# Performance work log

Measured on AMD Instinct MI355X. Metric: run time of the kernel, lower is better.

## Reference

```python
import jax, jax.numpy as jnp
import numpy as np

GH, GW, B, H, OUT = 9, 9, 1024, 256, 1


def setup_inputs() -> dict:
    key = jax.random.key(0)
    ks = jax.random.split(key, 16)
    N = GH * GW
    s3 = 1.0 / np.sqrt(3 * H)
    sH = 1.0 / np.sqrt(H)
    return {
        "x": jax.random.normal(ks[0], (B, GH, GW), jnp.float32),
        "h_ext": jax.random.normal(ks[1], (B, H), jnp.float32),
        "c_ext": jax.random.normal(ks[2], (B, H), jnp.float32),
        "grid_h": jax.random.normal(ks[3], (GH, GW, B, H), jnp.float32),
        "grid_c": jax.random.normal(ks[4], (GH, GW, B, H), jnp.float32),
        "W_hp": jax.random.normal(ks[5], (N, H, 3 * H), jnp.float32) * s3,
        "b_hp": jax.random.normal(ks[6], (N, H), jnp.float32) * s3,
        "W_cp": jax.random.normal(ks[7], (N, H, 3 * H), jnp.float32) * s3,
        "b_cp": jax.random.normal(ks[8], (N, H), jnp.float32) * s3,
        "W_ih": jax.random.normal(ks[9], (N, 4 * H, 1), jnp.float32) * sH,
        "W_hh": jax.random.normal(ks[10], (N, 4 * H, H), jnp.float32) * sH,
        "b_ih": jax.random.normal(ks[11], (N, 4 * H), jnp.float32) * sH,
        "b_hh": jax.random.normal(ks[12], (N, 4 * H), jnp.float32) * sH,
        "W_out": jax.random.normal(ks[13], (OUT, H), jnp.float32) * sH,
        "b_out": jnp.zeros((OUT,), jnp.float32),
    }


def _lstm_cell(x_cell, h0, c0, W_ih_k, W_hh_k, b_ih_k, b_hh_k):
    # x_cell: [B,1], h0/c0: [B,H]; torch LSTMCell math
    gates = x_cell @ W_ih_k.T + b_ih_k + h0 @ W_hh_k.T + b_hh_k  # [B,4H]
    i, f, g, o = jnp.split(gates, 4, axis=1)
    i, f, o = jax.nn.sigmoid(i), jax.nn.sigmoid(f), jax.nn.sigmoid(o)
    g = jnp.tanh(g)
    c = f * c0 + i * g
    h = o * jnp.tanh(c)
    return h, c


def reference(x, h_ext, c_ext, grid_h, grid_c,
              W_hp, b_hp, W_cp, b_cp,
              W_ih, W_hh, b_ih, b_hh, W_out, b_out):
    zeros = jnp.zeros((B, H), x.dtype)
    # new states, updated in raster order; left/up neighbors read NEW states
    new_h = [[None] * GW for _ in range(GH)]
    new_c = [[None] * GW for _ in range(GH)]
    for i in range(GH):
        for j in range(GW):
            k = i * GW + j
            h_prev, c_prev = grid_h[i, j], grid_c[i, j]
            if i == 0 and j == 0:
                h_left, c_left = h_ext, c_ext
            elif j > 0:
                h_left, c_left = new_h[i][j - 1], new_c[i][j - 1]
            else:
                h_left, c_left = zeros, zeros
            if i > 0:
                h_up, c_up = new_h[i - 1][j], new_c[i - 1][j]
            else:
                h_up, c_up = zeros, zeros
            comb_h = jnp.concatenate([h_left, h_up, h_prev], axis=1)  # [B,3H]
            comb_c = jnp.concatenate([c_left, c_up, c_prev], axis=1)
            ph = comb_h @ W_hp[k].T + b_hp[k]
            pc = comb_c @ W_cp[k].T + b_cp[k]
            x_cell = x[:, i, j][:, None]  # [B,1]
            h_new, c_new = _lstm_cell(x_cell, ph, pc, W_ih[k], W_hh[k], b_ih[k], b_hh[k])
            new_h[i][j], new_c[i][j] = h_new, c_new
    final_h, final_c = new_h[-1][-1], new_c[-1][-1]
    # fc_out with fc_layers_out=[0]: Linear + ReLU, then sigmoid
    out = jax.nn.sigmoid(jax.nn.relu(final_h @ W_out.T + b_out))
    gh = jnp.stack([jnp.stack(r, 0) for r in new_h], 0)
    gc = jnp.stack([jnp.stack(r, 0) for r in new_c], 0)
    return out, final_h, final_c, gh, gc
```

## Files before the change

kernel.cpp:

```cpp
#include <hip/hip_runtime.h>
#include <math.h>

#define BATCH 1024
#define HID 256
#define W3 768
#define SLOT (BATCH * HID)

typedef __bf16 bf16_t;
typedef __bf16 bf16x8 __attribute__((ext_vector_type(8)));
typedef __bf16 bf16x4 __attribute__((ext_vector_type(4)));
typedef float f32x4 __attribute__((ext_vector_type(4)));

__device__ inline bf16x8 cvt8(const float4 a, const float4 b) {
    bf16x8 r;
    r[0] = (bf16_t)a.x; r[1] = (bf16_t)a.y; r[2] = (bf16_t)a.z; r[3] = (bf16_t)a.w;
    r[4] = (bf16_t)b.x; r[5] = (bf16_t)b.y; r[6] = (bf16_t)b.z; r[7] = (bf16_t)b.w;
    return r;
}
__device__ inline bf16x4 cvt4(const float4 a) {
    bf16x4 r;
    r[0] = (bf16_t)a.x; r[1] = (bf16_t)a.y; r[2] = (bf16_t)a.z; r[3] = (bf16_t)a.w;
    return r;
}

__device__ inline int swz_work(int bid, int N) {
    const int xcd = bid & 7, idx = bid >> 3;
    const int q = N >> 3, r = N & 7;
    return (xcd < r ? xcd * (q + 1) : r * (q + 1) + (xcd - r) * q) + idx;
}

__global__ __launch_bounds__(256) void wcp_conv(
        const float* __restrict__ wcp, bf16_t* __restrict__ wcpb) {
    const size_t n4 = (size_t)81 * HID * W3 / 4;
    size_t i = (size_t)blockIdx.x * 256 + threadIdx.x;
    const size_t nth = (size_t)gridDim.x * 256;
    for (; i < n4; i += nth) {
        const float4 v = *(const float4*)(wcp + i * 4);
        *(bf16x4*)(wcpb + i * 4) = cvt4(v);
    }
}

__global__ __launch_bounds__(256) void whp_t_kernel(
        const float* __restrict__ whp, bf16_t* __restrict__ whpT) {
    const int k = blockIdx.z;
    const int m0 = blockIdx.x * 64, u0 = blockIdx.y * 64;
    const int t = threadIdx.x;
    const int tm = t & 63, tg = t >> 6;
    const float* src = whp + (size_t)k * HID * W3;
    bf16_t* dst = whpT + (size_t)k * W3 * HID;
    #pragma unroll
    for (int c = 0; c < 2; ++c) {
        const int ub = u0 + (tg + c * 4) * 8;
        bf16x8 v;
        #pragma unroll
        for (int i = 0; i < 8; ++i)
            v[i] = (bf16_t)src[(size_t)(ub + i) * W3 + m0 + tm];
        *(bf16x8*)(dst + (size_t)(m0 + tm) * HID + ub) = v;
    }
}

__global__ __launch_bounds__(256) void gvec_kernel(
        const float* __restrict__ Whh, const float* __restrict__ bhp,
        const float* __restrict__ bih, const float* __restrict__ bhh,
        float* __restrict__ gvec) {
    const int k = blockIdx.x, t = threadIdx.x;
    __shared__ float bsm[HID];
    bsm[t] = bhp[(size_t)k * HID + t];
    __syncthreads();
    #pragma unroll
    for (int g = 0; g < 4; ++g) {
        const int n4 = g * HID + t;
        const float* wr = Whh + (size_t)k * 4 * HID * HID + (size_t)n4 * HID;
        float s = 0.f;
        for (int u = 0; u < HID; u += 4) {
            const float4 w = *(const float4*)(wr + u);
            s += w.x * bsm[u] + w.y * bsm[u + 1] + w.z * bsm[u + 2] + w.w * bsm[u + 3];
        }
        gvec[(size_t)k * 1024 + n4] = s + bih[(size_t)k * 1024 + n4]
                                        + bhh[(size_t)k * 1024 + n4];
    }
}

__global__ __launch_bounds__(256) void compose_kernel(
        const float* __restrict__ Whh, const bf16_t* __restrict__ WhpT,
        bf16_t* __restrict__ CC) {
    __shared__ bf16_t As[128][40];
    __shared__ bf16_t Bs[128][40];
    const int work = swz_work(blockIdx.x, gridDim.x);
    const int k = work / 48, inner = work % 48;
    const int mt = inner % 6, by = inner / 6;
    const int m0 = mt * 128;
    const int t = threadIdx.x;
    const int lane = t & 63, wid = t >> 6;
    const int wm = wid & 1, wn = wid >> 1;
    const int ln = lane & 15, lh = lane >> 4;
    const int sr = t >> 1, sq = (t & 1) * 16;
    const int g_r = sr >> 5, du_r = sr & 31;
    const float* arow = Whh + (size_t)k * 1024 * HID
                        + (size_t)(g_r * HID + by * 32 + du_r) * HID + sq;
    const bf16_t* brow = WhpT + (size_t)k * W3 * HID + (size_t)(m0 + sr) * HID + sq;

    f32x4 acc[4][4] = {};
    for (int kb = 0; kb < 8; ++kb) {
        const float4 a0 = *(const float4*)(arow + kb * 32);
        const float4 a1 = *(const float4*)(arow + kb * 32 + 4);
        const float4 a2 = *(const float4*)(arow + kb * 32 + 8);
        const float4 a3 = *(const float4*)(arow + kb * 32 + 12);
        const bf16x8 bv0 = *(const bf16x8*)(brow + kb * 32);
        const bf16x8 bv1 = *(const bf16x8*)(brow + kb * 32 + 8);
        const bf16x8 av0 = cvt8(a0, a1), av1 = cvt8(a2, a3);
        __syncthreads();
        *(bf16x8*)&As[sr][sq] = av0;
        *(bf16x8*)&As[sr][sq + 8] = av1;
        *(bf16x8*)&Bs[sr][sq] = bv0;
        *(bf16x8*)&Bs[sr][sq + 8] = bv1;
        __syncthreads();
        bf16x8 af[4], bfv[4];
        #pragma unroll
        for (int mf = 0; mf < 4; ++mf)
            af[mf] = *(const bf16x8*)&Bs[wm * 64 + mf * 16 + ln][lh * 8];
        #pragma unroll
        for (int cf = 0; cf < 4; ++cf)
            bfv[cf] = *(const bf16x8*)&As[wn * 64 + cf * 16 + ln][lh * 8];
        #pragma unroll
        for (int mf = 0; mf < 4; ++mf)
            #pragma unroll
            for (int cf = 0; cf < 4; ++cf)
                acc[mf][cf] = __builtin_amdgcn_mfma_f32_16x16x32_bf16(
                    af[mf], bfv[cf], acc[mf][cf], 0, 0, 0);
    }
    bf16_t* outp = CC + (size_t)k * 1024 * W3;
    #pragma unroll
    for (int cf = 0; cf < 4; ++cf) {
        const int c = by * 128 + wn * 64 + cf * 16 + ln;
        #pragma unroll
        for (int mf = 0; mf < 4; ++mf) {
            const int m = m0 + wm * 64 + mf * 16 + lh * 4;
            bf16x4 v;
            #pragma unroll
            for (int r = 0; r < 4; ++r) v[r] = (bf16_t)acc[mf][cf][r];
            *(bf16x4*)(outp + (size_t)c * W3 + m) = v;
        }
    }
}

__global__ __launch_bounds__(256) void prevgates_kernel(
        const float* __restrict__ gridh, const float* __restrict__ gridc,
        const bf16_t* __restrict__ CC, const bf16_t* __restrict__ Wcpb,
        const float* __restrict__ gvec, const float* __restrict__ Wih,
        const float* __restrict__ bcp, const float* __restrict__ x,
        bf16_t* __restrict__ GP, bf16_t* __restrict__ PP) {
    __shared__ bf16_t A1[128][40];
    __shared__ bf16_t A2[128][40];
    __shared__ bf16_t B1[128][40];
    __shared__ bf16_t B2[32][40];
    const int work = swz_work(blockIdx.x, gridDim.x);
    const int k = work >> 6, inner = work & 63;
    const int bx = inner & 7, by = inner >> 3;
    const int t = threadIdx.x;
    const int lane = t & 63, wid = t >> 6;
    const int wm = wid & 1, wn = wid >> 1;
    const int ln = lane & 15, lh = lane >> 4;
    const int b0 = bx * 128, u0 = by * 32;
    const int sr = t >> 1, sq = (t & 1) * 16;
    const int du2 = t >> 3, kk4 = (t & 7) * 4;

    const float* ha = gridh + (size_t)k * SLOT + (size_t)(b0 + sr) * HID + sq;
    const float* ca = gridc + (size_t)k * SLOT + (size_t)(b0 + sr) * HID + sq;
    const bf16_t* b1r = CC + (size_t)k * 1024 * W3 + (size_t)(by * 128 + sr) * W3 + 512 + sq;
    const bf16_t* b2r = Wcpb + (size_t)k * HID * W3 + (size_t)(u0 + du2) * W3 + 512 + kk4;

    f32x4 accg[4][4] = {};
    f32x4 accp[4] = {};
    for (int kb = 0; kb < 8; ++kb) {
        const float4 h0 = *(const float4*)(ha + kb * 32);
        const float4 h1 = *(const float4*)(ha + kb * 32 + 4);
        const float4 h2 = *(const float4*)(ha + kb * 32 + 8);
        const float4 h3 = *(const float4*)(ha + kb * 32 + 12);
        const float4 c0 = *(const float4*)(ca + kb * 32);
        const float4 c1 = *(const float4*)(ca + kb * 32 + 4);
        const float4 c2 = *(const float4*)(ca + kb * 32 + 8);
        const float4 c3 = *(const float4*)(ca + kb * 32 + 12);
        const bf16x8 w0 = *(const bf16x8*)(b1r + kb * 32);
        const bf16x8 w1 = *(const bf16x8*)(b1r + kb * 32 + 8);
        const bf16x4 p0 = *(const bf16x4*)(b2r + kb * 32);
        const bf16x8 hv0 = cvt8(h0, h1), hv1 = cvt8(h2, h3);
        const bf16x8 cv0 = cvt8(c0, c1), cv1 = cvt8(c2, c3);
        __syncthreads();
        *(bf16x8*)&A1[sr][sq] = hv0;  *(bf16x8*)&A1[sr][sq + 8] = hv1;
        *(bf16x8*)&A2[sr][sq] = cv0;  *(bf16x8*)&A2[sr][sq + 8] = cv1;
        *(bf16x8*)&B1[sr][sq] = w0;   *(bf16x8*)&B1[sr][sq + 8] = w1;
        *(bf16x4*)&B2[du2][kk4] = p0;
        __syncthreads();
        bf16x8 af1[4], af2[4], bf1[4], bf2;
        #pragma unroll
        for (int mf = 0; mf < 4; ++mf) {
            af1[mf] = *(const bf16x8*)&A1[wm * 64 + mf * 16 + ln][lh * 8];
            af2[mf] = *(const bf16x8*)&A2[wm * 64 + mf * 16 + ln][lh * 8];
        }
        #pragma unroll
        for (int g = 0; g < 4; ++g)
            bf1[g] = *(const bf16x8*)&B1[g * 32 + wn * 16 + ln][lh * 8];
        bf2 = *(const bf16x8*)&B2[wn * 16 + ln][lh * 8];
        #pragma unroll
        for (int mf = 0; mf < 4; ++mf) {
            #pragma unroll
            for (int g = 0; g < 4; ++g)
                accg[mf][g] = __builtin_amdgcn_mfma_f32_16x16x32_bf16(
                    af1[mf], bf1[g], accg[mf][g], 0, 0, 0);
            accp[mf] = __builtin_amdgcn_mfma_f32_16x16x32_bf16(
                af2[mf], bf2, accp[mf], 0, 0, 0);
        }
    }

    const int u = u0 + wn * 16 + ln;
    float wv[4], gv[4];
    #pragma unroll
    for (int g = 0; g < 4; ++g) {
        const int n4 = g * HID + u;
        wv[g] = Wih[(size_t)k * 1024 + n4];
        gv[g] = gvec[(size_t)k * 1024 + n4];
    }
    const float bc = bcp[(size_t)k * HID + u];
    const int blk = by * 8 + bx;
    bf16_t* gpb = GP + (size_t)k * (BATCH * 1024) + (size_t)blk * 16384;
    bf16_t* ppb = PP + (size_t)k * SLOT + (size_t)blk * 4096;
    #pragma unroll
    for (int mf = 0; mf < 4; ++mf) {
        #pragma unroll
        for (int rp = 0; rp < 2; ++rp) {
            bf16x8 v;
            #pragma unroll
            for (int a = 0; a < 2; ++a) {
                const int r = rp * 2 + a;
                const int b = b0 + wm * 64 + mf * 16 + lh * 4 + r;
                const float xv = x[(size_t)b * 81 + k];
                #pragma unroll
                for (int g = 0; g < 4; ++g)
                    v[a * 4 + g] = (bf16_t)(accg[mf][g][r] + gv[g] + xv * wv[g]);
            }
            *(bf16x8*)(gpb + (size_t)(mf * 2 + rp) * 2048 + t * 8) = v;
        }
    }
    #pragma unroll
    for (int j = 0; j < 2; ++j) {
        bf16x8 v;
        #pragma unroll
        for (int h2 = 0; h2 < 2; ++h2) {
            const int mf = j * 2 + h2;
            #pragma unroll
            for (int r = 0; r < 4; ++r)
                v[h2 * 4 + r] = (bf16_t)(accp[mf][r] + bc);
        }
        *(bf16x8*)(ppb + (size_t)j * 2048 + t * 8) = v;
    }
}

struct Stage2Desc {
    const float* hs0; const float* cs0;
    const float* hs1; const float* cs1;
    const bf16_t* cc; const bf16_t* wcpb;
    const bf16_t* gp; const bf16_t* pp;
    float* gh; float* gc;
};
struct Stage2Args { Stage2Desc d[9]; };

__global__ __launch_bounds__(256) void stage2_kernel(Stage2Args args) {
    __shared__ bf16_t A1[128][40];
    __shared__ bf16_t A2[128][40];
    __shared__ bf16_t B1[128][40];
    __shared__ bf16_t B2[32][40];
    const int work = swz_work(blockIdx.x, gridDim.x);
    const int cell = work >> 6, inner = work & 63;
    const Stage2Desc sd = args.d[cell];
    const int bx = inner & 7, by = inner >> 3;
    const int t = threadIdx.x;
    const int lane = t & 63, wid = t >> 6;
    const int wm = wid & 1, wn = wid >> 1;
    const int ln = lane & 15, lh = lane >> 4;
    const int b0 = bx * 128, u0 = by * 32;
    const int sr = t >> 1, sq = (t & 1) * 16;
    const int du2 = t >> 3, kk4 = (t & 7) * 4;

    const int blk = by * 8 + bx;
    const bf16_t* gpb = sd.gp + (size_t)blk * 16384;
    const bf16_t* ppb = sd.pp + (size_t)blk * 4096;
    bf16x8 gpv[8], ppv[2];
    #pragma unroll
    for (int e = 0; e < 8; ++e)
        gpv[e] = *(const bf16x8*)(gpb + (size_t)e * 2048 + t * 8);
    #pragma unroll
    for (int j = 0; j < 2; ++j)
        ppv[j] = *(const bf16x8*)(ppb + (size_t)j * 2048 + t * 8);

    f32x4 accg[4][4] = {};
    f32x4 accp[4] = {};
    const float* hseg[2] = { sd.hs0, sd.hs1 };
    const float* cseg[2] = { sd.cs0, sd.cs1 };

    for (int s = 0; s < 2; ++s) {
        const float* hp = hseg[s];
        if (!hp) continue;
        const float* cp = cseg[s];
        const int ko = s * 256;
        const float* ha = hp + (size_t)(b0 + sr) * HID + sq;
        const float* ca = cp + (size_t)(b0 + sr) * HID + sq;
        const bf16_t* b1r = sd.cc + (size_t)(by * 128 + sr) * W3 + ko + sq;
        const bf16_t* b2r = sd.wcpb + (size_t)(u0 + du2) * W3 + ko + kk4;
        for (int kb = 0; kb < 8; ++kb) {
            const float4 h0 = *(const float4*)(ha + kb * 32);
            const float4 h1 = *(const float4*)(ha + kb * 32 + 4);
            const float4 h2 = *(const float4*)(ha + kb * 32 + 8);
            const float4 h3 = *(const float4*)(ha + kb * 32 + 12);
            const float4 c0 = *(const float4*)(ca + kb * 32);
            const float4 c1 = *(const float4*)(ca + kb * 32 + 4);
            const float4 c2 = *(const float4*)(ca + kb * 32 + 8);
            const float4 c3 = *(const float4*)(ca + kb * 32 + 12);
            const bf16x8 w0 = *(const bf16x8*)(b1r + kb * 32);
            const bf16x8 w1 = *(const bf16x8*)(b1r + kb * 32 + 8);
            const bf16x4 p0 = *(const bf16x4*)(b2r + kb * 32);
            const bf16x8 hv0 = cvt8(h0, h1), hv1 = cvt8(h2, h3);
            const bf16x8 cv0 = cvt8(c0, c1), cv1 = cvt8(c2, c3);
            __syncthreads();
            *(bf16x8*)&A1[sr][sq] = hv0;  *(bf16x8*)&A1[sr][sq + 8] = hv1;
            *(bf16x8*)&A2[sr][sq] = cv0;  *(bf16x8*)&A2[sr][sq + 8] = cv1;
            *(bf16x8*)&B1[sr][sq] = w0;   *(bf16x8*)&B1[sr][sq + 8] = w1;
            *(bf16x4*)&B2[du2][kk4] = p0;
            __syncthreads();
            bf16x8 af1[4], af2[4], bf1[4], bf2;
            #pragma unroll
            for (int mf = 0; mf < 4; ++mf) {
                af1[mf] = *(const bf16x8*)&A1[wm * 64 + mf * 16 + ln][lh * 8];
                af2[mf] = *(const bf16x8*)&A2[wm * 64 + mf * 16 + ln][lh * 8];
            }
            #pragma unroll
            for (int g = 0; g < 4; ++g)
                bf1[g] = *(const bf16x8*)&B1[g * 32 + wn * 16 + ln][lh * 8];
            bf2 = *(const bf16x8*)&B2[wn * 16 + ln][lh * 8];
            #pragma unroll
            for (int mf = 0; mf < 4; ++mf) {
                #pragma unroll
                for (int g = 0; g < 4; ++g)
                    accg[mf][g] = __builtin_amdgcn_mfma_f32_16x16x32_bf16(
                        af1[mf], bf1[g], accg[mf][g], 0, 0, 0);
                accp[mf] = __builtin_amdgcn_mfma_f32_16x16x32_bf16(
                    af2[mf], bf2, accp[mf], 0, 0, 0);
            }
        }
    }

    const int u = u0 + wn * 16 + ln;
    float pcv[4][4];
    #pragma unroll
    for (int j = 0; j < 2; ++j)
        #pragma unroll
        for (int h2 = 0; h2 < 2; ++h2)
            #pragma unroll
            for (int r = 0; r < 4; ++r)
                pcv[j * 2 + h2][r] = accp[j * 2 + h2][r] + (float)ppv[j][h2 * 4 + r];
    #pragma unroll
    for (int mf = 0; mf < 4; ++mf) {
        #pragma unroll
        for (int rp = 0; rp < 2; ++rp) {
            const bf16x8 v = gpv[mf * 2 + rp];
            #pragma unroll
            for (int a = 0; a < 2; ++a) {
                const int r = rp * 2 + a;
                const int b = b0 + wm * 64 + mf * 16 + lh * 4 + r;
                const float gi = accg[mf][0][r] + (float)v[a * 4 + 0];
                const float gf = accg[mf][1][r] + (float)v[a * 4 + 1];
                const float gg = accg[mf][2][r] + (float)v[a * 4 + 2];
                const float go = accg[mf][3][r] + (float)v[a * 4 + 3];
                const float pc = pcv[mf][r];
                const float i_ = 1.f / (1.f + expf(-gi));
                const float f_ = 1.f / (1.f + expf(-gf));
                const float o_ = 1.f / (1.f + expf(-go));
                const float g_ = tanhf(gg);
                const float cn = f_ * pc + i_ * g_;
                const float hn = o_ * tanhf(cn);
                sd.gh[(size_t)b * HID + u] = hn;
                sd.gc[(size_t)b * HID + u] = cn;
            }
        }
    }
}

__global__ __launch_bounds__(256) void final_kernel(
        const float* __restrict__ gh88, const float* __restrict__ gc88,
        const float* __restrict__ Wout, const float* __restrict__ bout,
        float* __restrict__ out, float* __restrict__ fh, float* __restrict__ fc) {
    const int tid = blockIdx.x * blockDim.x + threadIdx.x;
    const int nth = gridDim.x * blockDim.x;
    for (int idx = tid; idx < BATCH * HID; idx += nth) {
        fh[idx] = gh88[idx];
        fc[idx] = gc88[idx];
    }
    if (tid < BATCH) {
        float s = bout[0];
        for (int k = 0; k < HID; ++k) s += gh88[(size_t)tid * HID + k] * Wout[k];
        s = fmaxf(s, 0.f);
        out[tid] = 1.f / (1.f + expf(-s));
    }
}

template<bool ATOMIC>
__device__ __forceinline__ void proj_core(
        const float* __restrict__ src, const float* __restrict__ W, int koff,
        const float* __restrict__ bias, float* __restrict__ out,
        bf16_t (*Asm)[40], bf16_t (*Bsm)[40]) {
    const int t = threadIdx.x;
    const int lane = t & 63, wid = t >> 6;
    const int wm = wid & 1, wn = wid >> 1;
    const int ln = lane & 15, lh = lane >> 4;
    const int b0 = blockIdx.x * 128, n0 = blockIdx.y * 128;
    const int sr = t >> 1, sq = (t & 1) * 16;
    const float* arow = src + (size_t)(b0 + sr) * HID + sq;
    const float* wrow = W + (size_t)(n0 + sr) * W3 + koff + sq;
    f32x4 acc[4][4] = {};
    for (int kb = 0; kb < 8; ++kb) {
        const float4 a0 = *(const float4*)(arow + kb * 32);
        const float4 a1 = *(const float4*)(arow + kb * 32 + 4);
        const float4 a2 = *(const float4*)(arow + kb * 32 + 8);
        const float4 a3 = *(const float4*)(arow + kb * 32 + 12);
        const float4 w0 = *(const float4*)(wrow + kb * 32);
        const float4 w1 = *(const float4*)(wrow + kb * 32 + 4);
        const float4 w2 = *(const float4*)(wrow + kb * 32 + 8);
        const float4 w3 = *(const float4*)(wrow + kb * 32 + 12);
        const bf16x8 av0 = cvt8(a0, a1), av1 = cvt8(a2, a3);
        const bf16x8 bv0 = cvt8(w0, w1), bv1 = cvt8(w2, w3);
        __syncthreads();
        *(bf16x8*)&Asm[sr][sq] = av0;
        *(bf16x8*)&Asm[sr][sq + 8] = av1;
        *(bf16x8*)&Bsm[sr][sq] = bv0;
        *(bf16x8*)&Bsm[sr][sq + 8] = bv1;
        __syncthreads();
        bf16x8 af[4], bfv[4];
        #pragma unroll
        for (int mf = 0; mf < 4; ++mf)
            af[mf] = *(const bf16x8*)&Asm[wm * 64 + mf * 16 + ln][lh * 8];
        #pragma unroll
        for (int nf = 0; nf < 4; ++nf)
            bfv[nf] = *(const bf16x8*)&Bsm[wn * 64 + nf * 16 + ln][lh * 8];
        #pragma unroll
        for (int mf = 0; mf < 4; ++mf)
            #pragma unroll
            for (int nf = 0; nf < 4; ++nf)
                acc[mf][nf] = __builtin_amdgcn_mfma_f32_16x16x32_bf16(
                    af[mf], bfv[nf], acc[mf][nf], 0, 0, 0);
    }
    #pragma unroll
    for (int nf = 0; nf < 4; ++nf) {
        const int n = n0 + wn * 64 + nf * 16 + ln;
        const float bn = ATOMIC ? 0.f : bias[n];
        #pragma unroll
        for (int mf = 0; mf < 4; ++mf)
            #pragma unroll
            for (int r = 0; r < 4; ++r) {
                const int b = b0 + wm * 64 + mf * 16 + lh * 4 + r;
                if (ATOMIC)
                    unsafeAtomicAdd(out + (size_t)b * HID + n, acc[mf][nf][r]);
                else
                    out[(size_t)b * HID + n] = acc[mf][nf][r] + bn;
            }
    }
}

struct SegDesc { const float* src; const float* W; const float* bias; float* out; int koff; };
struct SegArgs { SegDesc d[36]; };

__global__ __launch_bounds__(256) void projseg_kernel(SegArgs a) {
    __shared__ bf16_t As[128][40];
    __shared__ bf16_t Bs[128][40];
    const SegDesc d = a.d[blockIdx.z];
    if (d.bias) proj_core<false>(d.src, d.W, d.koff, d.bias, d.out, As, Bs);
    else        proj_core<true>(d.src, d.W, d.koff, nullptr, d.out, As, Bs);
}

struct CellDesc {
    const float* ph; const float* pc;
    const float* Whh; const float* Wih; const float* bih; const float* bhh;
    const float* xcol;
    float* gh; float* gc;
};
struct CellBatchArgs { CellDesc d[9]; };

__global__ __launch_bounds__(256) void cell_kernel(CellBatchArgs args) {
    const CellDesc cd = args.d[blockIdx.z];
    __shared__ bf16_t Psm[128][40];
    __shared__ bf16_t Wsm[128][40];
    const int t = threadIdx.x;
    const int lane = t & 63, wid = t >> 6;
    const int wm = wid & 1, wn = wid >> 1;
    const int ln = lane & 15, lh = lane >> 4;
    const int b0 = blockIdx.x * 128;
    const int u0 = blockIdx.y * 32;
    const int sr = t >> 1, sq = (t & 1) * 16;
    const float* prow = cd.ph + (size_t)(b0 + sr) * HID + sq;
    const int cg = sr >> 5, cdu = sr & 31;
    const float* wrow = cd.Whh + (size_t)(cg * HID + u0 + cdu) * HID + sq;
    f32x4 acc[4][4] = {};
    for (int kb = 0; kb < 8; ++kb) {
        const float4 p0 = *(const float4*)(prow + kb * 32);
        const float4 p1 = *(const float4*)(prow + kb * 32 + 4);
        const float4 p2 = *(const float4*)(prow + kb * 32 + 8);
        const float4 p3 = *(const float4*)(prow + kb * 32 + 12);
        const float4 w0 = *(const float4*)(wrow + kb * 32);
        const float4 w1 = *(const float4*)(wrow + kb * 32 + 4);
        const float4 w2 = *(const float4*)(wrow + kb * 32 + 8);
        const float4 w3 = *(const float4*)(wrow + kb * 32 + 12);
        const bf16x8 pv0 = cvt8(p0, p1), pv1 = cvt8(p2, p3);
        const bf16x8 wv0 = cvt8(w0, w1), wv1 = cvt8(w2, w3);
        __syncthreads();
        *(bf16x8*)&Psm[sr][sq] = pv0;
        *(bf16x8*)&Psm[sr][sq + 8] = pv1;
        *(bf16x8*)&Wsm[sr][sq] = wv0;
        *(bf16x8*)&Wsm[sr][sq + 8] = wv1;
        __syncthreads();
        bf16x8 af[4], bfr[4];
        #pragma unroll
        for (int mf = 0; mf < 4; ++mf)
            af[mf] = *(const bf16x8*)&Psm[wm * 64 + mf * 16 + ln][lh * 8];
        #pragma unroll
        for (int g = 0; g < 4; ++g)
            bfr[g] = *(const bf16x8*)&Wsm[g * 32 + wn * 16 + ln][lh * 8];
        #pragma unroll
        for (int mf = 0; mf < 4; ++mf)
            #pragma unroll
            for (int g = 0; g < 4; ++g)
                acc[mf][g] = __builtin_amdgcn_mfma_f32_16x16x32_bf16(
                    af[mf], bfr[g], acc[mf][g], 0, 0, 0);
    }
    const int u = u0 + wn * 16 + ln;
    float wih[4], bsum[4];
    #pragma unroll
    for (int g = 0; g < 4; ++g) {
        const int n = g * HID + u;
        wih[g] = cd.Wih[n];
        bsum[g] = cd.bih[n] + cd.bhh[n];
    }
    #pragma unroll
    for (int mf = 0; mf < 4; ++mf)
        #pragma unroll
        for (int r = 0; r < 4; ++r) {
            const int b = b0 + wm * 64 + mf * 16 + lh * 4 + r;
            const float xv = cd.xcol[(size_t)b * 81];
            const float gi = acc[mf][0][r] + xv * wih[0] + bsum[0];
            const float gf = acc[mf][1][r] + xv * wih[1] + bsum[1];
            const float gg = acc[mf][2][r] + xv * wih[2] + bsum[2];
            const float go = acc[mf][3][r] + xv * wih[3] + bsum[3];
            const float i_ = 1.f / (1.f + expf(-gi));
            const float f_ = 1.f / (1.f + expf(-gf));
            const float o_ = 1.f / (1.f + expf(-go));
            const float g_ = tanhf(gg);
            const float c0 = cd.pc[(size_t)b * HID + u];
            const float cn = f_ * c0 + i_ * g_;
            const float hn = o_ * tanhf(cn);
            cd.gh[(size_t)b * HID + u] = hn;
            cd.gc[(size_t)b * HID + u] = cn;
        }
}

extern "C" void kernel_launch(void* const* d_in, const int* in_sizes, int n_in,
                              void* d_out, int out_size, void* d_ws, size_t ws_size,
                              hipStream_t stream) {
    const float* x      = (const float*)d_in[0];
    const float* h_ext  = (const float*)d_in[1];
    const float* c_ext  = (const float*)d_in[2];
    const float* grid_h = (const float*)d_in[3];
    const float* grid_c = (const float*)d_in[4];
    const float* W_hp   = (const float*)d_in[5];
    const float* b_hp   = (const float*)d_in[6];
    const float* W_cp   = (const float*)d_in[7];
    const float* b_cp   = (const float*)d_in[8];
    const float* W_ih   = (const float*)d_in[9];
    const float* W_hh   = (const float*)d_in[10];
    const float* b_ih   = (const float*)d_in[11];
    const float* b_hh   = (const float*)d_in[12];
    const float* W_out  = (const float*)d_in[13];
    const float* b_out  = (const float*)d_in[14];

    float* out = (float*)d_out;
    float* fh  = out + BATCH * 1;
    float* fc  = fh + SLOT;
    float* gh  = fc + SLOT;
    float* gc  = gh + (size_t)81 * SLOT;

    const size_t wt_b  = (size_t)81 * W3 * HID * 2;
    const size_t wcp_b = (size_t)81 * HID * W3 * 2;
    const size_t cc_b  = (size_t)81 * 1024 * W3 * 2;
    const size_t gp_b  = (size_t)81 * BATCH * 1024 * 2;
    const size_t pp_b  = (size_t)81 * SLOT * 2;
    const size_t gv_b  = (size_t)81 * 1024 * 4;
    const size_t need = wt_b + wcp_b + cc_b + gp_b + pp_b + gv_b;

    if (ws_size >= need) {
        char* p = (char*)d_ws;
        bf16_t* WhpT = (bf16_t*)p; p += wt_b;
        bf16_t* Wcpb = (bf16_t*)p; p += wcp_b;
        bf16_t* CC   = (bf16_t*)p; p += cc_b;
        bf16_t* GP   = (bf16_t*)p; p += gp_b;
        bf16_t* PP   = (bf16_t*)p; p += pp_b;
        float*  gvec = (float*)p;

        wcp_conv<<<dim3(2048), 256, 0, stream>>>(W_cp, Wcpb);
        whp_t_kernel<<<dim3(12, 4, 81), 256, 0, stream>>>(W_hp, WhpT);
        gvec_kernel<<<dim3(81), 256, 0, stream>>>(W_hh, b_hp, b_ih, b_hh, gvec);
        compose_kernel<<<dim3(81 * 48), 256, 0, stream>>>(W_hh, WhpT, CC);
        prevgates_kernel<<<dim3(81 * 64), 256, 0, stream>>>(
            grid_h, grid_c, CC, Wcpb, gvec, W_ih, b_cp, x, GP, PP);

        for (int d = 0; d <= 16; ++d) {
            const int i_lo = d > 8 ? d - 8 : 0;
            const int i_hi = d < 8 ? d : 8;
            const int nc = i_hi - i_lo + 1;
            Stage2Args sa{};
            for (int s = 0; s < nc; ++s) {
                const int i = i_lo + s, j = d - i;
                const int k = i * 9 + j;
                const float *hl = nullptr, *cl = nullptr, *hu = nullptr, *cu = nullptr;
                if (i == 0 && j == 0)      { hl = h_ext; cl = c_ext; }
                else if (j > 0)            { hl = gh + (size_t)(k - 1) * SLOT;
                                             cl = gc + (size_t)(k - 1) * SLOT; }
                if (i > 0)                 { hu = gh + (size_t)(k - 9) * SLOT;
                                             cu = gc + (size_t)(k - 9) * SLOT; }
                sa.d[s] = { hl, cl, hu, cu,
                            CC + (size_t)k * 1024 * W3,
                            Wcpb + (size_t)k * HID * W3,
                            GP + (size_t)k * BATCH * 1024,
                            PP + (size_t)k * SLOT,
                            gh + (size_t)k * SLOT, gc + (size_t)k * SLOT };
            }
            stage2_kernel<<<dim3(nc * 64), 256, 0, stream>>>(sa);
        }
    } else {
        float* ws = (float*)d_ws;
        for (int d = 0; d <= 16; ++d) {
            const int i_lo = d > 8 ? d - 8 : 0;
            const int i_hi = d < 8 ? d : 8;
            const int nc = i_hi - i_lo + 1;
            SegArgs base{}, inc{};
            CellBatchArgs ca{};
            int nb = 0, ni = 0;
            for (int s = 0; s < nc; ++s) {
                const int i = i_lo + s, j = d - i;
                const int k = i * 9 + j;
                float* oh = ws + (size_t)(2 * s) * SLOT;
                float* oc = oh + SLOT;
                const float* Wh = W_hp + (size_t)k * HID * W3;
                const float* Wc = W_cp + (size_t)k * HID * W3;
                base.d[nb++] = { grid_h + (size_t)k * SLOT, Wh, b_hp + (size_t)k * HID, oh, 512 };
                base.d[nb++] = { grid_c + (size_t)k * SLOT, Wc, b_cp + (size_t)k * HID, oc, 512 };
                if (i == 0 && j == 0) {
                    inc.d[ni++] = { h_ext, Wh, nullptr, oh, 0 };
                    inc.d[ni++] = { c_ext, Wc, nullptr, oc, 0 };
                } else if (j > 0) {
                    inc.d[ni++] = { gh + (size_t)(k - 1) * SLOT, Wh, nullptr, oh, 0 };
                    inc.d[ni++] = { gc + (size_t)(k - 1) * SLOT, Wc, nullptr, oc, 0 };
                }
                if (i > 0) {
                    inc.d[ni++] = { gh + (size_t)(k - 9) * SLOT, Wh, nullptr, oh, 256 };
                    inc.d[ni++] = { gc + (size_t)(k - 9) * SLOT, Wc, nullptr, oc, 256 };
                }
                ca.d[s] = { oh, oc,
                            W_hh + (size_t)k * 4 * HID * HID,
                            W_ih + (size_t)k * 4 * HID,
                            b_ih + (size_t)k * 4 * HID,
                            b_hh + (size_t)k * 4 * HID,
                            x + i * 9 + j,
                            gh + (size_t)k * SLOT,
                            gc + (size_t)k * SLOT };
            }
            projseg_kernel<<<dim3(8, 2, nb), 256, 0, stream>>>(base);
            projseg_kernel<<<dim3(8, 2, ni), 256, 0, stream>>>(inc);
            cell_kernel<<<dim3(8, 8, nc), 256, 0, stream>>>(ca);
        }
    }
    final_kernel<<<dim3(64), 256, 0, stream>>>(
        gh + (size_t)80 * SLOT, gc + (size_t)80 * SLOT,
        W_out, b_out, out, fh, fc);
}
```

Measured before the change: 1.151 ms.

## Fuse compose, prevgates and wavefront stages into one persistent dataflow kernel

Result: slower. 3.988 ms (+246.4%).

```diff
diff --git a/kernel.cpp b/kernel.cpp
--- a/kernel.cpp
+++ b/kernel.cpp
@@ -5,6 +5,11 @@
 #define HID 256
 #define W3 768
 #define SLOT (BATCH * HID)
+
+#define NJC (81 * 48)
+#define NJP (NJC + 81 * 64)
+#define NJT (NJP + 81 * 64)
+#define NBLK 768
 
 typedef __bf16 bf16_t;
 typedef __bf16 bf16x8 __attribute__((ext_vector_type(8)));
@@ -21,12 +26,6 @@
     bf16x4 r;
     r[0] = (bf16_t)a.x; r[1] = (bf16_t)a.y; r[2] = (bf16_t)a.z; r[3] = (bf16_t)a.w;
     return r;
-}
-
-__device__ inline int swz_work(int bid, int N) {
-    const int xcd = bid & 7, idx = bid >> 3;
-    const int q = N >> 3, r = N & 7;
-    return (xcd < r ? xcd * (q + 1) : r * (q + 1) + (xcd - r) * q) + idx;
 }
 
 __global__ __launch_bounds__(256) void wcp_conv(
@@ -81,306 +80,316 @@
     }
 }
 
-__global__ __launch_bounds__(256) void compose_kernel(
-        const float* __restrict__ Whh, const bf16_t* __restrict__ WhpT,
-        bf16_t* __restrict__ CC) {
-    __shared__ bf16_t As[128][40];
-    __shared__ bf16_t Bs[128][40];
-    const int work = swz_work(blockIdx.x, gridDim.x);
-    const int k = work / 48, inner = work % 48;
-    const int mt = inner % 6, by = inner / 6;
-    const int m0 = mt * 128;
+__global__ __launch_bounds__(256) void zero_flags(int* __restrict__ f) {
+    if (threadIdx.x < 243) f[threadIdx.x] = 0;
+}
+
+struct MegaArgs {
+    const float* h_ext; const float* c_ext;
+    const float* grid_h; const float* grid_c;
+    const float* Whh; const bf16_t* WhpT; const bf16_t* Wcpb;
+    const float* gvec; const float* Wih; const float* bcp; const float* x;
+    bf16_t* CC; bf16_t* GP; bf16_t* PP;
+    float* gh; float* gc;
+    int* Fc; int* Fp; int* Fs;
+    int cellorder[81];
+};
+
+__global__ __launch_bounds__(256, 4) void mega_kernel(MegaArgs a) {
+    __shared__ __align__(16) char smem_raw[33280];
+    bf16_t (*A1)[40] = (bf16_t(*)[40])(smem_raw);
+    bf16_t (*A2)[40] = (bf16_t(*)[40])(smem_raw + 10240);
+    bf16_t (*B1)[40] = (bf16_t(*)[40])(smem_raw + 20480);
+    bf16_t (*B2)[40] = (bf16_t(*)[40])(smem_raw + 30720);
+
     const int t = threadIdx.x;
     const int lane = t & 63, wid = t >> 6;
     const int wm = wid & 1, wn = wid >> 1;
     const int ln = lane & 15, lh = lane >> 4;
     const int sr = t >> 1, sq = (t & 1) * 16;
-    const int g_r = sr >> 5, du_r = sr & 31;
-    const float* arow = Whh + (size_t)k * 1024 * HID
-                        + (size_t)(g_r * HID + by * 32 + du_r) * HID + sq;
-    const bf16_t* brow = WhpT + (size_t)k * W3 * HID + (size_t)(m0 + sr) * HID + sq;
-
-    f32x4 acc[4][4] = {};
-    for (int kb = 0; kb < 8; ++kb) {
-        const float4 a0 = *(const float4*)(arow + kb * 32);
-        const float4 a1 = *(const float4*)(arow + kb * 32 + 4);
-        const float4 a2 = *(const float4*)(arow + kb * 32 + 8);
-        const float4 a3 = *(const float4*)(arow + kb * 32 + 12);
-        const bf16x8 bv0 = *(const bf16x8*)(brow + kb * 32);
-        const bf16x8 bv1 = *(const bf16x8*)(brow + kb * 32 + 8);
-        const bf16x8 av0 = cvt8(a0, a1), av1 = cvt8(a2, a3);
-        __syncthreads();
-        *(bf16x8*)&As[sr][sq] = av0;
-        *(bf16x8*)&As[sr][sq + 8] = av1;
-        *(bf16x8*)&Bs[sr][sq] = bv0;
-        *(bf16x8*)&Bs[sr][sq + 8] = bv1;
-        __syncthreads();
-        bf16x8 af[4], bfv[4];
-        #pragma unroll
-        for (int mf = 0; mf < 4; ++mf)
-            af[mf] = *(const bf16x8*)&Bs[wm * 64 + mf * 16 + ln][lh * 8];
-        #pragma unroll
-        for (int cf = 0; cf < 4; ++cf)
-            bfv[cf] = *(const bf16x8*)&As[wn * 64 + cf * 16 + ln][lh * 8];
-        #pragma unroll
-        for (int mf = 0; mf < 4; ++mf)
-            #pragma unroll
-            for (int cf = 0; cf < 4; ++cf)
-                acc[mf][cf] = __builtin_amdgcn_mfma_f32_16x16x32_bf16(
-                    af[mf], bfv[cf], acc[mf][cf], 0, 0, 0);
-    }
-    bf16_t* outp = CC + (size_t)k * 1024 * W3;
-    #pragma unroll
-    for (int cf = 0; cf < 4; ++cf) {
-        const int c = by * 128 + wn * 64 + cf * 16 + ln;
-        #pragma unroll
-        for (int mf = 0; mf < 4; ++mf) {
-            const int m = m0 + wm * 64 + mf * 16 + lh * 4;
-            bf16x4 v;
-            #pragma unroll
-            for (int r = 0; r < 4; ++r) v[r] = (bf16_t)acc[mf][cf][r];
-            *(bf16x4*)(outp + (size_t)c * W3 + m) = v;
-        }
-    }
-}
-
-__global__ __launch_bounds__(256) void prevgates_kernel(
-        const float* __restrict__ gridh, const float* __restrict__ gridc,
-        const bf16_t* __restrict__ CC, const bf16_t* __restrict__ Wcpb,
-        const float* __restrict__ gvec, const float* __restrict__ Wih,
-        const float* __restrict__ bcp, const float* __restrict__ x,
-        bf16_t* __restrict__ GP, bf16_t* __restrict__ PP) {
-    __shared__ bf16_t A1[128][40];
-    __shared__ bf16_t A2[128][40];
-    __shared__ bf16_t B1[128][40];
-    __shared__ bf16_t B2[32][40];
-    const int work = swz_work(blockIdx.x, gridDim.x);
-    const int k = work >> 6, inner = work & 63;
-    const int bx = inner & 7, by = inner >> 3;
-    const int t = threadIdx.x;
-    const int lane = t & 63, wid = t >> 6;
-    const int wm = wid & 1, wn = wid >> 1;
-    const int ln = lane & 15, lh = lane >> 4;
-    const int b0 = bx * 128, u0 = by * 32;
-    const int sr = t >> 1, sq = (t & 1) * 16;
     const int du2 = t >> 3, kk4 = (t & 7) * 4;
 
-    const float* ha = gridh + (size_t)k * SLOT + (size_t)(b0 + sr) * HID + sq;
-    const float* ca = gridc + (size_t)k * SLOT + (size_t)(b0 + sr) * HID + sq;
-    const bf16_t* b1r = CC + (size_t)k * 1024 * W3 + (size_t)(by * 128 + sr) * W3 + 512 + sq;
-    const bf16_t* b2r = Wcpb + (size_t)k * HID * W3 + (size_t)(u0 + du2) * W3 + 512 + kk4;
-
-    f32x4 accg[4][4] = {};
-    f32x4 accp[4] = {};
-    for (int kb = 0; kb < 8; ++kb) {
-        const float4 h0 = *(const float4*)(ha + kb * 32);
-        const float4 h1 = *(const float4*)(ha + kb * 32 + 4);
-        const float4 h2 = *(const float4*)(ha + kb * 32 + 8);
-        const float4 h3 = *(const float4*)(ha + kb * 32 + 12);
-        const float4 c0 = *(const float4*)(ca + kb * 32);
-        const float4 c1 = *(const float4*)(ca + kb * 32 + 4);
-        const float4 c2 = *(const float4*)(ca + kb * 32 + 8);
-        const float4 c3 = *(const float4*)(ca + kb * 32 + 12);
-        const bf16x8 w0 = *(const bf16x8*)(b1r + kb * 32);
-        const bf16x8 w1 = *(const bf16x8*)(b1r + kb * 32 + 8);
-        const bf16x4 p0 = *(const bf16x4*)(b2r + kb * 32);
-        const bf16x8 hv0 = cvt8(h0, h1), hv1 = cvt8(h2, h3);
-        const bf16x8 cv0 = cvt8(c0, c1), cv1 = cvt8(c2, c3);
-        __syncthreads();
-        *(bf16x8*)&A1[sr][sq] = hv0;  *(bf16x8*)&A1[sr][sq + 8] = hv1;
-        *(bf16x8*)&A2[sr][sq] = cv0;  *(bf16x8*)&A2[sr][sq + 8] = cv1;
-        *(bf16x8*)&B1[sr][sq] = w0;   *(bf16x8*)&B1[sr][sq + 8] = w1;
-        *(bf16x4*)&B2[du2][kk4] = p0;
-        __syncthreads();
-        bf16x8 af1[4], af2[4], bf1[4], bf2;
-        #pragma unroll
-        for (int mf = 0; mf < 4; ++mf) {
-            af1[mf] = *(const bf16x8*)&A1[wm * 64 + mf * 16 + ln][lh * 8];
-            af2[mf] = *(const bf16x8*)&A2[wm * 64 + mf * 16 + ln][lh * 8];
-        }
-        #pragma unroll
-        for (int g = 0; g < 4; ++g)
-            bf1[g] = *(const bf16x8*)&B1[g * 32 + wn * 16 + ln][lh * 8];
-        bf2 = *(const bf16x8*)&B2[wn * 16 + ln][lh * 8];
-        #pragma unroll
-        for (int mf = 0; mf < 4; ++mf) {
-            #pragma unroll
-            for (int g = 0; g < 4; ++g)
-                accg[mf][g] = __builtin_amdgcn_mfma_f32_16x16x32_bf16(
-                    af1[mf], bf1[g], accg[mf][g], 0, 0, 0);
-            accp[mf] = __builtin_amdgcn_mfma_f32_16x16x32_bf16(
-                af2[mf], bf2, accp[mf], 0, 0, 0);
-        }
-    }
-
-    const int u = u0 + wn * 16 + ln;
-    float wv[4], gv[4];
-    #pragma unroll
-    for (int g = 0; g < 4; ++g) {
-        const int n4 = g * HID + u;
-        wv[g] = Wih[(size_t)k * 1024 + n4];
-        gv[g] = gvec[(size_t)k * 1024 + n4];
-    }
-    const float bc = bcp[(size_t)k * HID + u];
-    const int blk = by * 8 + bx;
-    bf16_t* gpb = GP + (size_t)k * (BATCH * 1024) + (size_t)blk * 16384;
-    bf16_t* ppb = PP + (size_t)k * SLOT + (size_t)blk * 4096;
-    #pragma unroll
-    for (int mf = 0; mf < 4; ++mf) {
-        #pragma unroll
-        for (int rp = 0; rp < 2; ++rp) {
-            bf16x8 v;
-            #pragma unroll
-            for (int a = 0; a < 2; ++a) {
-                const int r = rp * 2 + a;
-                const int b = b0 + wm * 64 + mf * 16 + lh * 4 + r;
-                const float xv = x[(size_t)b * 81 + k];
+    for (int j = blockIdx.x; j < NJT; j += NBLK) {
+        if (j < NJC) {
+            const int r = j / 48, inner = j % 48;
+            const int k = a.cellorder[r];
+            const int mt = inner % 6, by = inner / 6;
+            const int m0 = mt * 128;
+            const int g_r = sr >> 5, du_r = sr & 31;
+            const float* arow = a.Whh + (size_t)k * 1024 * HID
+                                + (size_t)(g_r * HID + by * 32 + du_r) * HID + sq;
+            const bf16_t* brow = a.WhpT + (size_t)k * W3 * HID + (size_t)(m0 + sr) * HID + sq;
+            f32x4 acc[4][4] = {};
+            for (int kb = 0; kb < 8; ++kb) {
+                const float4 a0 = *(const float4*)(arow + kb * 32);
+                const float4 a1 = *(const float4*)(arow + kb * 32 + 4);
+                const float4 a2 = *(const float4*)(arow + kb * 32 + 8);
+                const float4 a3 = *(const float4*)(arow + kb * 32 + 12);
+                const bf16x8 bv0 = *(const bf16x8*)(brow + kb * 32);
+                const bf16x8 bv1 = *(const bf16x8*)(brow + kb * 32 + 8);
+                const bf16x8 av0 = cvt8(a0, a1), av1 = cvt8(a2, a3);
+                __syncthreads();
+                *(bf16x8*)&A1[sr][sq] = av0;
+                *(bf16x8*)&A1[sr][sq + 8] = av1;
+                *(bf16x8*)&B1[sr][sq] = bv0;
+                *(bf16x8*)&B1[sr][sq + 8] = bv1;
+                __syncthreads();
+                bf16x8 af[4], bfv[4];
+                #pragma unroll
+                for (int mf = 0; mf < 4; ++mf)
+                    af[mf] = *(const bf16x8*)&B1[wm * 64 + mf * 16 + ln][lh * 8];
+                #pragma unroll
+                for (int cf = 0; cf < 4; ++cf)
+                    bfv[cf] = *(const bf16x8*)&A1[wn * 64 + cf * 16 + ln][lh * 8];
+                #pragma unroll
+                for (int mf = 0; mf < 4; ++mf)
+                    #pragma unroll
+                    for (int cf = 0; cf < 4; ++cf)
+                        acc[mf][cf] = __builtin_amdgcn_mfma_f32_16x16x32_bf16(
+                            af[mf], bfv[cf], acc[mf][cf], 0, 0, 0);
+            }
+            bf16_t* outp = a.CC + (size_t)k * 1024 * W3;
+            #pragma unroll
+            for (int cf = 0; cf < 4; ++cf) {
+                const int c = by * 128 + wn * 64 + cf * 16 + ln;
+                #pragma unroll
+                for (int mf = 0; mf < 4; ++mf) {
+                    const int m = m0 + wm * 64 + mf * 16 + lh * 4;
+                    bf16x4 v;
+                    #pragma unroll
+                    for (int rr = 0; rr < 4; ++rr) v[rr] = (bf16_t)acc[mf][cf][rr];
+                    *(bf16x4*)(outp + (size_t)c * W3 + m) = v;
+                }
+            }
+            __syncthreads();
+            if (t == 0)
+                __hip_atomic_fetch_add(a.Fc + k, 1, __ATOMIC_RELEASE, __HIP_MEMORY_SCOPE_AGENT);
+        } else if (j < NJP) {
+            const int r = (j - NJC) >> 6, tile = (j - NJC) & 63;
+            const int k = a.cellorder[r];
+            const int bx = tile & 7, by = tile >> 3;
+            const int b0 = bx * 128, u0 = by * 32;
+            if (t == 0) {
+                while (__hip_atomic_load(a.Fc + k, __ATOMIC_RELAXED, __HIP_MEMORY_SCOPE_AGENT) < 48)
+                    __builtin_amdgcn_s_sleep(8);
+                __hip_atomic_load(a.Fc + k, __ATOMIC_ACQUIRE, __HIP_MEMORY_SCOPE_AGENT);
+            }
+            __syncthreads();
+            __threadfence();
+
+            const float* ha = a.grid_h + (size_t)k * SLOT + (size_t)(b0 + sr) * HID + sq;
+            const float* ca = a.grid_c + (size_t)k * SLOT + (size_t)(b0 + sr) * HID + sq;
+            const bf16_t* b1r = a.CC + (size_t)k * 1024 * W3 + (size_t)(by * 128 + sr) * W3 + 512 + sq;
+            const bf16_t* b2r = a.Wcpb + (size_t)k * HID * W3 + (size_t)(u0 + du2) * W3 + 512 + kk4;
+            f32x4 accg[4][4] = {};
+            f32x4 accp[4] = {};
+            for (int kb = 0; kb < 8; ++kb) {
+                const float4 h0 = *(const float4*)(ha + kb * 32);
+                const float4 h1 = *(const float4*)(ha + kb * 32 + 4);
+                const float4 h2 = *(const float4*)(ha + kb * 32 + 8);
+                const float4 h3 = *(const float4*)(ha + kb * 32 + 12);
+                const float4 c0 = *(const float4*)(ca + kb * 32);
+                const float4 c1 = *(const float4*)(ca + kb * 32 + 4);
+                const float4 c2 = *(const float4*)(ca + kb * 32 + 8);
+                const float4 c3 = *(const float4*)(ca + kb * 32 + 12);
+                const bf16x8 w0 = *(const bf16x8*)(b1r + kb * 32);
+                const bf16x8 w1 = *(const bf16x8*)(b1r + kb * 32 + 8);
+                const bf16x4 p0 = *(const bf16x4*)(b2r + kb * 32);
+                const bf16x8 hv0 = cvt8(h0, h1), hv1 = cvt8(h2, h3);
+                const bf16x8 cv0 = cvt8(c0, c1), cv1 = cvt8(c2, c3);
+                __syncthreads();
+                *(bf16x8*)&A1[sr][sq] = hv0;  *(bf16x8*)&A1[sr][sq + 8] = hv1;
+                *(bf16x8*)&A2[sr][sq] = cv0;  *(bf16x8*)&A2[sr][sq + 8] = cv1;
+                *(bf16x8*)&B1[sr][sq] = w0;   *(bf16x8*)&B1[sr][sq + 8] = w1;
+                *(bf16x4*)&B2[du2][kk4] = p0;
+                __syncthreads();
+                bf16x8 af1[4], af2[4], bf1[4], bf2;
+                #pragma unroll
+                for (int mf = 0; mf < 4; ++mf) {
+                    af1[mf] = *(const bf16x8*)&A1[wm * 64 + mf * 16 + ln][lh * 8];
+                    af2[mf] = *(const bf16x8*)&A2[wm * 64 + mf * 16 + ln][lh * 8];
+                }
                 #pragma unroll
                 for (int g = 0; g < 4; ++g)
-                    v[a * 4 + g] = (bf16_t)(accg[mf][g][r] + gv[g] + xv * wv[g]);
-            }
-            *(bf16x8*)(gpb + (size_t)(mf * 2 + rp) * 2048 + t * 8) = v;
-        }
-    }
-    #pragma unroll
-    for (int j = 0; j < 2; ++j) {
-        bf16x8 v;
-        #pragma unroll
-        for (int h2 = 0; h2 < 2; ++h2) {
-            const int mf = j * 2 + h2;
-            #pragma unroll
-            for (int r = 0; r < 4; ++r)
-                v[h2 * 4 + r] = (bf16_t)(accp[mf][r] + bc);
-        }
-        *(bf16x8*)(ppb + (size_t)j * 2048 + t * 8) = v;
-    }
-}
-
-struct Stage2Desc {
-    const float* hs0; const float* cs0;
-    const float* hs1; const float* cs1;
-    const bf16_t* cc; const bf16_t* wcpb;
-    const bf16_t* gp; const bf16_t* pp;
-    float* gh; float* gc;
-};
-struct Stage2Args { Stage2Desc d[9]; };
-
-__global__ __launch_bounds__(256) void stage2_kernel(Stage2Args args) {
-    __shared__ bf16_t A1[128][40];
-    __shared__ bf16_t A2[128][40];
-    __shared__ bf16_t B1[128][40];
-    __shared__ bf16_t B2[32][40];
-    const int work = swz_work(blockIdx.x, gridDim.x);
-    const int cell = work >> 6, inner = work & 63;
-    const Stage2Desc sd = args.d[cell];
-    const int bx = inner & 7, by = inner >> 3;
-    const int t = threadIdx.x;
-    const int lane = t & 63, wid = t >> 6;
-    const int wm = wid & 1, wn = wid >> 1;
-    const int ln = lane & 15, lh = lane >> 4;
-    const int b0 = bx * 128, u0 = by * 32;
-    const int sr = t >> 1, sq = (t & 1) * 16;
-    const int du2 = t >> 3, kk4 = (t & 7) * 4;
-
-    const int blk = by * 8 + bx;
-    const bf16_t* gpb = sd.gp + (size_t)blk * 16384;
-    const bf16_t* ppb = sd.pp + (size_t)blk * 4096;
-    bf16x8 gpv[8], ppv[2];
-    #pragma unroll
-    for (int e = 0; e < 8; ++e)
-        gpv[e] = *(const bf16x8*)(gpb + (size_t)e * 2048 + t * 8);
-    #pragma unroll
-    for (int j = 0; j < 2; ++j)
-        ppv[j] = *(const bf16x8*)(ppb + (size_t)j * 2048 + t * 8);
-
-    f32x4 accg[4][4] = {};
-    f32x4 accp[4] = {};
-    const float* hseg[2] = { sd.hs0, sd.hs1 };
-    const float* cseg[2] = { sd.cs0, sd.cs1 };
-
-    for (int s = 0; s < 2; ++s) {
-        const float* hp = hseg[s];
-        if (!hp) continue;
-        const float* cp = cseg[s];
-        const int ko = s * 256;
-        const float* ha = hp + (size_t)(b0 + sr) * HID + sq;
-        const float* ca = cp + (size_t)(b0 + sr) * HID + sq;
-        const bf16_t* b1r = sd.cc + (size_t)(by * 128 + sr) * W3 + ko + sq;
-        const bf16_t* b2r = sd.wcpb + (size_t)(u0 + du2) * W3 + ko + kk4;
-        for (int kb = 0; kb < 8; ++kb) {
-            const float4 h0 = *(const float4*)(ha + kb * 32);
-            const float4 h1 = *(const float4*)(ha + kb * 32 + 4);
-            const float4 h2 = *(const float4*)(ha + kb * 32 + 8);
-            const float4 h3 = *(const float4*)(ha + kb * 32 + 12);
-            const float4 c0 = *(const float4*)(ca + kb * 32);
-            const float4 c1 = *(const float4*)(ca + kb * 32 + 4);
-            const float4 c2 = *(const float4*)(ca + kb * 32 + 8);
-            const float4 c3 = *(const float4*)(ca + kb * 32 + 12);
-            const bf16x8 w0 = *(const bf16x8*)(b1r + kb * 32);
-            const bf16x8 w1 = *(const bf16x8*)(b1r + kb * 32 + 8);
-            const bf16x4 p0 = *(const bf16x4*)(b2r + kb * 32);
-            const bf16x8 hv0 = cvt8(h0, h1), hv1 = cvt8(h2, h3);
-            const bf16x8 cv0 = cvt8(c0, c1), cv1 = cvt8(c2, c3);
+                    bf1[g] = *(const bf16x8*)&B1[g * 32 + wn * 16 + ln][lh * 8];
+                bf2 = *(const bf16x8*)&B2[wn * 16 + ln][lh * 8];
+                #pragma unroll
+                for (int mf = 0; mf < 4; ++mf) {
+                    #pragma unroll
+                    for (int g = 0; g < 4; ++g)
+                        accg[mf][g] = __builtin_amdgcn_mfma_f32_16x16x32_bf16(
+                            af1[mf], bf1[g], accg[mf][g], 0, 0, 0);
+                    accp[mf] = __builtin_amdgcn_mfma_f32_16x16x32_bf16(
+                        af2[mf], bf2, accp[mf], 0, 0, 0);
+                }
+            }
+            const int u = u0 + wn * 16 + ln;
+            float wv[4], gv[4];
+            #pragma unroll
+            for (int g = 0; g < 4; ++g) {
+                const int n4 = g * HID + u;
+                wv[g] = a.Wih[(size_t)k * 1024 + n4];
+                gv[g] = a.gvec[(size_t)k * 1024 + n4];
+            }
+            const float bc = a.bcp[(size_t)k * HID + u];
+            bf16_t* gpb = a.GP + (size_t)k * (BATCH * 1024) + (size_t)tile * 16384;
+            bf16_t* ppb = a.PP + (size_t)k * SLOT + (size_t)tile * 4096;
+            #pragma unroll
+            for (int mf = 0; mf < 4; ++mf) {
+                #pragma unroll
+                for (int rp = 0; rp < 2; ++rp) {
+                    bf16x8 v;
+                    #pragma unroll
+                    for (int aa = 0; aa < 2; ++aa) {
+                        const int rr = rp * 2 + aa;
+                        const int b = b0 + wm * 64 + mf * 16 + lh * 4 + rr;
+                        const float xv = a.x[(size_t)b * 81 + k];
+                        #pragma unroll
+                        for (int g = 0; g < 4; ++g)
+                            v[aa * 4 + g] = (bf16_t)(accg[mf][g][rr] + gv[g] + xv * wv[g]);
+                    }
+                    *(bf16x8*)(gpb + (size_t)(mf * 2 + rp) * 2048 + t * 8) = v;
+                }
+            }
+            #pragma unroll
+            for (int jj = 0; jj < 2; ++jj) {
+                bf16x8 v;
+                #pragma unroll
+                for (int h2 = 0; h2 < 2; ++h2) {
+                    const int mf = jj * 2 + h2;
+                    #pragma unroll
+                    for (int rr = 0; rr < 4; ++rr)
+                        v[h2 * 4 + rr] = (bf16_t)(accp[mf][rr] + bc);
+                }
+                *(bf16x8*)(ppb + (size_t)jj * 2048 + t * 8) = v;
+            }
             __syncthreads();
-            *(bf16x8*)&A1[sr][sq] = hv0;  *(bf16x8*)&A1[sr][sq + 8] = hv1;
-            *(bf16x8*)&A2[sr][sq] = cv0;  *(bf16x8*)&A2[sr][sq + 8] = cv1;
-            *(bf16x8*)&B1[sr][sq] = w0;   *(bf16x8*)&B1[sr][sq + 8] = w1;
-            *(bf16x4*)&B2[du2][kk4] = p0;
+            if (t == 0)
+                __hip_atomic_fetch_add(a.Fp + k, 1, __ATOMIC_RELEASE, __HIP_MEMORY_SCOPE_AGENT);
+        } else {
+            const int r = (j - NJP) >> 6, tile = (j - NJP) & 63;
+            const int k = a.cellorder[r];
+            const int ci = k / 9, cj = k % 9;
+            const int bx = tile & 7, by = tile >> 3;
+            const int b0 = bx * 128, u0 = by * 32;
+            const int depL = (cj > 0) ? (k - 1) : -1;
+            const int depU = (ci > 0) ? (k - 9) : -1;
+            if (t == 0) {
+                for (;;) {
+                    bool ok = __hip_atomic_load(a.Fc + k, __ATOMIC_RELAXED, __HIP_MEMORY_SCOPE_AGENT) >= 48
+                           && __hip_atomic_load(a.Fp + k, __ATOMIC_RELAXED, __HIP_MEMORY_SCOPE_AGENT) >= 64;
+                    if (ok && depL >= 0)
+                        ok = __hip_atomic_load(a.Fs + depL, __ATOMIC_RELAXED, __HIP_MEMORY_SCOPE_AGENT) >= 64;
+                    if (ok && depU >= 0)
+                        ok = __hip_atomic_load(a.Fs + depU, __ATOMIC_RELAXED, __HIP_MEMORY_SCOPE_AGENT) >= 64;
+                    if (ok) break;
+                    __builtin_amdgcn_s_sleep(8);
+                }
+                __hip_atomic_load(a.Fp + k, __ATOMIC_ACQUIRE, __HIP_MEMORY_SCOPE_AGENT);
+            }
             __syncthreads();
-            bf16x8 af1[4], af2[4], bf1[4], bf2;
+            __threadfence();
+
+            const float *hl = nullptr, *cl = nullptr, *hu = nullptr, *cu = nullptr;
+            if (ci == 0 && cj == 0) { hl = a.h_ext; cl = a.c_ext; }
+            else if (cj > 0) { hl = a.gh + (size_t)(k - 1) * SLOT; cl = a.gc + (size_t)(k - 1) * SLOT; }
+            if (ci > 0) { hu = a.gh + (size_t)(k - 9) * SLOT; cu = a.gc + (size_t)(k - 9) * SLOT; }
+            const float* hseg[2] = { hl, hu };
+            const float* cseg[2] = { cl, cu };
+
+            f32x4 accg[4][4] = {};
+            f32x4 accp[4] = {};
+            for (int s = 0; s < 2; ++s) {
+                const float* hp = hseg[s];
+                if (!hp) continue;
+                const float* cp = cseg[s];
+                const int ko = s * 256;
+                const float* ha = hp + (size_t)(b0 + sr) * HID + sq;
+                const float* ca = cp + (size_t)(b0 + sr) * HID + sq;
+                const bf16_t* b1r = a.CC + (size_t)k * 1024 * W3 + (size_t)(by * 128 + sr) * W3 + ko + sq;
+                const bf16_t* b2r = a.Wcpb + (size_t)k * HID * W3 + (size_t)(u0 + du2) * W3 + ko + kk4;
+                for (int kb = 0; kb < 8; ++kb) {
+                    const float4 h0 = *(const float4*)(ha + kb * 32);
+                    const float4 h1 = *(const float4*)(ha + kb * 32 + 4);
+                    const float4 h2 = *(const float4*)(ha + kb * 32 + 8);
+                    const float4 h3 = *(const float4*)(ha + kb * 32 + 12);
+                    const float4 c0 = *(const float4*)(ca + kb * 32);
+                    const float4 c1 = *(const float4*)(ca + kb * 32 + 4);
+                    const float4 c2 = *(const float4*)(ca + kb * 32 + 8);
+                    const float4 c3 = *(const float4*)(ca + kb * 32 + 12);
+                    const bf16x8 w0 = *(const bf16x8*)(b1r + kb * 32);
+                    const bf16x8 w1 = *(const bf16x8*)(b1r + kb * 32 + 8);
+                    const bf16x4 p0 = *(const bf16x4*)(b2r + kb * 32);
+                    const bf16x8 hv0 = cvt8(h0, h1), hv1 = cvt8(h2, h3);
+                    const bf16x8 cv0 = cvt8(c0, c1), cv1 = cvt8(c2, c3);
+                    __syncthreads();
+                    *(bf16x8*)&A1[sr][sq] = hv0;  *(bf16x8*)&A1[sr][sq + 8] = hv1;
+                    *(bf16x8*)&A2[sr][sq] = cv0;  *(bf16x8*)&A2[sr][sq + 8] = cv1;
+                    *(bf16x8*)&B1[sr][sq] = w0;   *(bf16x8*)&B1[sr][sq + 8] = w1;
+                    *(bf16x4*)&B2[du2][kk4] = p0;
+                    __syncthreads();
+                    bf16x8 af1[4], af2[4], bf1[4], bf2;
+                    #pragma unroll
+                    for (int mf = 0; mf < 4; ++mf) {
+                        af1[mf] = *(const bf16x8*)&A1[wm * 64 + mf * 16 + ln][lh * 8];
+                        af2[mf] = *(const bf16x8*)&A2[wm * 64 + mf * 16 + ln][lh * 8];
+                    }
+                    #pragma unroll
+                    for (int g = 0; g < 4; ++g)
+                        bf1[g] = *(const bf16x8*)&B1[g * 32 + wn * 16 + ln][lh * 8];
+                    bf2 = *(const bf16x8*)&B2[wn * 16 + ln][lh * 8];
+                    #pragma unroll
+                    for (int mf = 0; mf < 4; ++mf) {
+                        #pragma unroll
+                        for (int g = 0; g < 4; ++g)
+                            accg[mf][g] = __builtin_amdgcn_mfma_f32_16x16x32_bf16(
+                                af1[mf], bf1[g], accg[mf][g], 0, 0, 0);
+                        accp[mf] = __builtin_amdgcn_mfma_f32_16x16x32_bf16(
+                            af2[mf], bf2, accp[mf], 0, 0, 0);
+                    }
+                }
+            }
+            const int u = u0 + wn * 16 + ln;
+            const bf16_t* gpb = a.GP + (size_t)k * (BATCH * 1024) + (size_t)tile * 16384;
+            const bf16_t* ppb = a.PP + (size_t)k * SLOT + (size_t)tile * 4096;
+            float pcv[4][4];
+            #pragma unroll
+            for (int jj = 0; jj < 2; ++jj) {
+                const bf16x8 v = *(const bf16x8*)(ppb + (size_t)jj * 2048 + t * 8);
+                #pragma unroll
+                for (int h2 = 0; h2 < 2; ++h2)
+                    #pragma unroll
+                    for (int rr = 0; rr < 4; ++rr)
+                        pcv[jj * 2 + h2][rr] = accp[jj * 2 + h2][rr] + (float)v[h2 * 4 + rr];
+            }
             #pragma unroll
             for (int mf = 0; mf < 4; ++mf) {
-                af1[mf] = *(const bf16x8*)&A1[wm * 64 + mf * 16 + ln][lh * 8];
-                af2[mf] = *(const bf16x8*)&A2[wm * 64 + mf * 16 + ln][lh * 8];
-            }
-            #pragma unroll
-            for (int g = 0; g < 4; ++g)
-                bf1[g] = *(const bf16x8*)&B1[g * 32 + wn * 16 + ln][lh * 8];
-            bf2 = *(const bf16x8*)&B2[wn * 16 + ln][lh * 8];
-            #pragma unroll
-            for (int mf = 0; mf < 4; ++mf) {
-                #pragma unroll
-                for (int g = 0; g < 4; ++g)
-                    accg[mf][g] = __builtin_amdgcn_mfma_f32_16x16x32_bf16(
-                        af1[mf], bf1[g], accg[mf][g], 0, 0, 0);
-                accp[mf] = __builtin_amdgcn_mfma_f32_16x16x32_bf16(
-                    af2[mf], bf2, accp[mf], 0, 0, 0);
-            }
-        }
-    }
-
-    const int u = u0 + wn * 16 + ln;
-    float pcv[4][4];
-    #pragma unroll
-    for (int j = 0; j < 2; ++j)
-        #pragma unroll
-        for (int h2 = 0; h2 < 2; ++h2)
-            #pragma unroll
-            for (int r = 0; r < 4; ++r)
-                pcv[j * 2 + h2][r] = accp[j * 2 + h2][r] + (float)ppv[j][h2 * 4 + r];
-    #pragma unroll
-    for (int mf = 0; mf < 4; ++mf) {
-        #pragma unroll
-        for (int rp = 0; rp < 2; ++rp) {
-            const bf16x8 v = gpv[mf * 2 + rp];
-            #pragma unroll
-            for (int a = 0; a < 2; ++a) {
-                const int r = rp * 2 + a;
-                const int b = b0 + wm * 64 + mf * 16 + lh * 4 + r;
-                const float gi = accg[mf][0][r] + (float)v[a * 4 + 0];
-                const float gf = accg[mf][1][r] + (float)v[a * 4 + 1];
-                const float gg = accg[mf][2][r] + (float)v[a * 4 + 2];
-                const float go = accg[mf][3][r] + (float)v[a * 4 + 3];
-                const float pc = pcv[mf][r];
-                const float i_ = 1.f / (1.f + expf(-gi));
-                const float f_ = 1.f / (1.f + expf(-gf));
-                const float o_ = 1.f / (1.f + expf(-go));
-                const float g_ = tanhf(gg);
-                const float cn = f_ * pc + i_ * g_;
-                const float hn = o_ * tanhf(cn);
-                sd.gh[(size_t)b * HID + u] = hn;
-                sd.gc[(size_t)b * HID + u] = cn;
-            }
+                #pragma unroll
+                for (int rp = 0; rp < 2; ++rp) {
+                    const bf16x8 v = *(const bf16x8*)(gpb + (size_t)(mf * 2 + rp) * 2048 + t * 8);
+                    #pragma unroll
+                    for (int aa = 0; aa < 2; ++aa) {
+                        const int rr = rp * 2 + aa;
+                        const int b = b0 + wm * 64 + mf * 16 + lh * 4 + rr;
+                        const float gi = accg[mf][0][rr] + (float)v[aa * 4 + 0];
+                        const float gf = accg[mf][1][rr] + (float)v[aa * 4 + 1];
+                        const float gg = accg[mf][2][rr] + (float)v[aa * 4 + 2];
+                        const float go = accg[mf][3][rr] + (float)v[aa * 4 + 3];
+                        const float pc = pcv[mf][rr];
+                        const float i_ = 1.f / (1.f + expf(-gi));
+                        const float f_ = 1.f / (1.f + expf(-gf));
+                        const float o_ = 1.f / (1.f + expf(-go));
+                        const float g_ = tanhf(gg);
+                        const float cn = f_ * pc + i_ * g_;
+                        const float hn = o_ * tanhf(cn);
+                        a.gh[(size_t)(k * SLOT + (size_t)b * HID + u)] = hn;
+                        a.gc[(size_t)(k * SLOT + (size_t)b * HID + u)] = cn;
+                    }
+                }
+            }
+            __syncthreads();
+            if (t == 0)
+                __hip_atomic_fetch_add(a.Fs + k, 1, __ATOMIC_RELEASE, __HIP_MEMORY_SCOPE_AGENT);
         }
     }
 }
@@ -401,163 +410,6 @@
         s = fmaxf(s, 0.f);
         out[tid] = 1.f / (1.f + expf(-s));
     }
-}
-
-template<bool ATOMIC>
-__device__ __forceinline__ void proj_core(
-        const float* __restrict__ src, const float* __restrict__ W, int koff,
-        const float* __restrict__ bias, float* __restrict__ out,
-        bf16_t (*Asm)[40], bf16_t (*Bsm)[40]) {
-    const int t = threadIdx.x;
-    const int lane = t & 63, wid = t >> 6;
-    const int wm = wid & 1, wn = wid >> 1;
-    const int ln = lane & 15, lh = lane >> 4;
-    const int b0 = blockIdx.x * 128, n0 = blockIdx.y * 128;
-    const int sr = t >> 1, sq = (t & 1) * 16;
-    const float* arow = src + (size_t)(b0 + sr) * HID + sq;
-    const float* wrow = W + (size_t)(n0 + sr) * W3 + koff + sq;
-    f32x4 acc[4][4] = {};
-    for (int kb = 0; kb < 8; ++kb) {
-        const float4 a0 = *(const float4*)(arow + kb * 32);
-        const float4 a1 = *(const float4*)(arow + kb * 32 + 4);
-        const float4 a2 = *(const float4*)(arow + kb * 32 + 8);
-        const float4 a3 = *(const float4*)(arow + kb * 32 + 12);
-        const float4 w0 = *(const float4*)(wrow + kb * 32);
-        const float4 w1 = *(const float4*)(wrow + kb * 32 + 4);
-        const float4 w2 = *(const float4*)(wrow + kb * 32 + 8);
-        const float4 w3 = *(const float4*)(wrow + kb * 32 + 12);
-        const bf16x8 av0 = cvt8(a0, a1), av1 = cvt8(a2, a3);
-        const bf16x8 bv0 = cvt8(w0, w1), bv1 = cvt8(w2, w3);
-        __syncthreads();
-        *(bf16x8*)&Asm[sr][sq] = av0;
-        *(bf16x8*)&Asm[sr][sq + 8] = av1;
-        *(bf16x8*)&Bsm[sr][sq] = bv0;
-        *(bf16x8*)&Bsm[sr][sq + 8] = bv1;
-        __syncthreads();
-        bf16x8 af[4], bfv[4];
-        #pragma unroll
-        for (int mf = 0; mf < 4; ++mf)
-            af[mf] = *(const bf16x8*)&Asm[wm * 64 + mf * 16 + ln][lh * 8];
-        #pragma unroll
-        for (int nf = 0; nf < 4; ++nf)
-            bfv[nf] = *(const bf16x8*)&Bsm[wn * 64 + nf * 16 + ln][lh * 8];
-        #pragma unroll
-        for (int mf = 0; mf < 4; ++mf)
-            #pragma unroll
-            for (int nf = 0; nf < 4; ++nf)
-                acc[mf][nf] = __builtin_amdgcn_mfma_f32_16x16x32_bf16(
-                    af[mf], bfv[nf], acc[mf][nf], 0, 0, 0);
-    }
-    #pragma unroll
-    for (int nf = 0; nf < 4; ++nf) {
-        const int n = n0 + wn * 64 + nf * 16 + ln;
-        const float bn = ATOMIC ? 0.f : bias[n];
-        #pragma unroll
-        for (int mf = 0; mf < 4; ++mf)
-            #pragma unroll
-            for (int r = 0; r < 4; ++r) {
-                const int b = b0 + wm * 64 + mf * 16 + lh * 4 + r;
-                if (ATOMIC)
-                    unsafeAtomicAdd(out + (size_t)b * HID + n, acc[mf][nf][r]);
-                else
-                    out[(size_t)b * HID + n] = acc[mf][nf][r] + bn;
-            }
-    }
-}
-
-struct SegDesc { const float* src; const float* W; const float* bias; float* out; int koff; };
-struct SegArgs { SegDesc d[36]; };
-
-__global__ __launch_bounds__(256) void projseg_kernel(SegArgs a) {
-    __shared__ bf16_t As[128][40];
-    __shared__ bf16_t Bs[128][40];
-    const SegDesc d = a.d[blockIdx.z];
-    if (d.bias) proj_core<false>(d.src, d.W, d.koff, d.bias, d.out, As, Bs);
-    else        proj_core<true>(d.src, d.W, d.koff, nullptr, d.out, As, Bs);
-}
-
-struct CellDesc {
-    const float* ph; const float* pc;
-    const float* Whh; const float* Wih; const float* bih; const float* bhh;
-    const float* xcol;
-    float* gh; float* gc;
-};
-struct CellBatchArgs { CellDesc d[9]; };
-
-__global__ __launch_bounds__(256) void cell_kernel(CellBatchArgs args) {
-    const CellDesc cd = args.d[blockIdx.z];
-    __shared__ bf16_t Psm[128][40];
-    __shared__ bf16_t Wsm[128][40];
-    const int t = threadIdx.x;
-    const int lane = t & 63, wid = t >> 6;
-    const int wm = wid & 1, wn = wid >> 1;
-    const int ln = lane & 15, lh = lane >> 4;
-    const int b0 = blockIdx.x * 128;
-    const int u0 = blockIdx.y * 32;
-    const int sr = t >> 1, sq = (t & 1) * 16;
-    const float* prow = cd.ph + (size_t)(b0 + sr) * HID + sq;
-    const int cg = sr >> 5, cdu = sr & 31;
-    const float* wrow = cd.Whh + (size_t)(cg * HID + u0 + cdu) * HID + sq;
-    f32x4 acc[4][4] = {};
-    for (int kb = 0; kb < 8; ++kb) {
-        const float4 p0 = *(const float4*)(prow + kb * 32);
-        const float4 p1 = *(const float4*)(prow + kb * 32 + 4);
-        const float4 p2 = *(const float4*)(prow + kb * 32 + 8);
-        const float4 p3 = *(const float4*)(prow + kb * 32 + 12);
-        const float4 w0 = *(const float4*)(wrow + kb * 32);
-        const float4 w1 = *(const float4*)(wrow + kb * 32 + 4);
-        const float4 w2 = *(const float4*)(wrow + kb * 32 + 8);
-        const float4 w3 = *(const float4*)(wrow + kb * 32 + 12);
-        const bf16x8 pv0 = cvt8(p0, p1), pv1 = cvt8(p2, p3);
-        const bf16x8 wv0 = cvt8(w0, w1), wv1 = cvt8(w2, w3);
-        __syncthreads();
-        *(bf16x8*)&Psm[sr][sq] = pv0;
-        *(bf16x8*)&Psm[sr][sq + 8] = pv1;
-        *(bf16x8*)&Wsm[sr][sq] = wv0;
-        *(bf16x8*)&Wsm[sr][sq + 8] = wv1;
-        __syncthreads();
-        bf16x8 af[4], bfr[4];
-        #pragma unroll
-        for (int mf = 0; mf < 4; ++mf)
-            af[mf] = *(const bf16x8*)&Psm[wm * 64 + mf * 16 + ln][lh * 8];
-        #pragma unroll
-        for (int g = 0; g < 4; ++g)
-            bfr[g] = *(const bf16x8*)&Wsm[g * 32 + wn * 16 + ln][lh * 8];
-        #pragma unroll
-        for (int mf = 0; mf < 4; ++mf)
-            #pragma unroll
-            for (int g = 0; g < 4; ++g)
-                acc[mf][g] = __builtin_amdgcn_mfma_f32_16x16x32_bf16(
-                    af[mf], bfr[g], acc[mf][g], 0, 0, 0);
-    }
-    const int u = u0 + wn * 16 + ln;
-    float wih[4], bsum[4];
-    #pragma unroll
-    for (int g = 0; g < 4; ++g) {
-        const int n = g * HID + u;
-        wih[g] = cd.Wih[n];
-        bsum[g] = cd.bih[n] + cd.bhh[n];
-    }
-    #pragma unroll
-    for (int mf = 0; mf < 4; ++mf)
-        #pragma unroll
-        for (int r = 0; r < 4; ++r) {
-            const int b = b0 + wm * 64 + mf * 16 + lh * 4 + r;
-            const float xv = cd.xcol[(size_t)b * 81];
-            const float gi = acc[mf][0][r] + xv * wih[0] + bsum[0];
-            const float gf = acc[mf][1][r] + xv * wih[1] + bsum[1];
-            const float gg = acc[mf][2][r] + xv * wih[2] + bsum[2];
-            const float go = acc[mf][3][r] + xv * wih[3] + bsum[3];
-            const float i_ = 1.f / (1.f + expf(-gi));
-            const float f_ = 1.f / (1.f + expf(-gf));
-            const float o_ = 1.f / (1.f + expf(-go));
-            const float g_ = tanhf(gg);
-            const float c0 = cd.pc[(size_t)b * HID + u];
-            const float cn = f_ * c0 + i_ * g_;
-            const float hn = o_ * tanhf(cn);
-            cd.gh[(size_t)b * HID + u] = hn;
-            cd.gc[(size_t)b * HID + u] = cn;
-        }
 }
 
 extern "C" void kernel_launch(void* const* d_in, const int* in_sizes, int n_in,
@@ -591,90 +443,44 @@
     const size_t gp_b  = (size_t)81 * BATCH * 1024 * 2;
     const size_t pp_b  = (size_t)81 * SLOT * 2;
     const size_t gv_b  = (size_t)81 * 1024 * 4;
-    const size_t need = wt_b + wcp_b + cc_b + gp_b + pp_b + gv_b;
-
-    if (ws_size >= need) {
-        char* p = (char*)d_ws;
-        bf16_t* WhpT = (bf16_t*)p; p += wt_b;
-        bf16_t* Wcpb = (bf16_t*)p; p += wcp_b;
-        bf16_t* CC   = (bf16_t*)p; p += cc_b;
-        bf16_t* GP   = (bf16_t*)p; p += gp_b;
-        bf16_t* PP   = (bf16_t*)p; p += pp_b;
-        float*  gvec = (float*)p;
-
-        wcp_conv<<<dim3(2048), 256, 0, stream>>>(W_cp, Wcpb);
-        whp_t_kernel<<<dim3(12, 4, 81), 256, 0, stream>>>(W_hp, WhpT);
-        gvec_kernel<<<dim3(81), 256, 0, stream>>>(W_hh, b_hp, b_ih, b_hh, gvec);
-        compose_kernel<<<dim3(81 * 48), 256, 0, stream>>>(W_hh, WhpT, CC);
-        prevgates_kernel<<<dim3(81 * 64), 256, 0, stream>>>(
-            grid_h, grid_c, CC, Wcpb, gvec, W_ih, b_cp, x, GP, PP);
-
+    const size_t fl_b  = 1024;
+    const size_t need = wt_b + wcp_b + cc_b + gp_b + pp_b + gv_b + fl_b;
+
+    char* p = (char*)d_ws;
+    bf16_t* WhpT = (bf16_t*)p; p += wt_b;
+    bf16_t* Wcpb = (bf16_t*)p; p += wcp_b;
+    bf16_t* CC   = (bf16_t*)p; p += cc_b;
+    bf16_t* GP   = (bf16_t*)p; p += gp_b;
+    bf16_t* PP   = (bf16_t*)p; p += pp_b;
+    float*  gvec = (float*)p;  p += gv_b;
+    int*    flags = (int*)p;
+
+    (void)need; (void)ws_size;
+
+    wcp_conv<<<dim3(2048), 256, 0, stream>>>(W_cp, Wcpb);
+    whp_t_kernel<<<dim3(12, 4, 81), 256, 0, stream>>>(W_hp, WhpT);
+    gvec_kernel<<<dim3(81), 256, 0, stream>>>(W_hh, b_hp, b_ih, b_hh, gvec);
+    zero_flags<<<dim3(1), 256, 0, stream>>>(flags);
+
+    MegaArgs ma;
+    ma.h_ext = h_ext; ma.c_ext = c_ext;
+    ma.grid_h = grid_h; ma.grid_c = grid_c;
+    ma.Whh = W_hh; ma.WhpT = WhpT; ma.Wcpb = Wcpb;
+    ma.gvec = gvec; ma.Wih = W_ih; ma.bcp = b_cp; ma.x = x;
+    ma.CC = CC; ma.GP = GP; ma.PP = PP;
+    ma.gh = gh; ma.gc = gc;
+    ma.Fc = flags; ma.Fp = flags + 81; ma.Fs = flags + 162;
+    {
+        int idx = 0;
         for (int d = 0; d <= 16; ++d) {
             const int i_lo = d > 8 ? d - 8 : 0;
             const int i_hi = d < 8 ? d : 8;
-            const int nc = i_hi - i_lo + 1;
-            Stage2Args sa{};
-            for (int s = 0; s < nc; ++s) {
-                const int i = i_lo + s, j = d - i;
-                const int k = i * 9 + j;
-                const float *hl = nullptr, *cl = nullptr, *hu = nullptr, *cu = nullptr;
-                if (i == 0 && j == 0)      { hl = h_ext; cl = c_ext; }
-                else if (j > 0)            { hl = gh + (size_t)(k - 1) * SLOT;
-                                             cl = gc + (size_t)(k - 1) * SLOT; }
-                if (i > 0)                 { hu = gh + (size_t)(k - 9) * SLOT;
-                                             cu = gc + (size_t)(k - 9) * SLOT; }
-                sa.d[s] = { hl, cl, hu, cu,
-                            CC + (size_t)k * 1024 * W3,
-                            Wcpb + (size_t)k * HID * W3,
-                            GP + (size_t)k * BATCH * 1024,
-                            PP + (size_t)k * SLOT,
-                            gh + (size_t)k * SLOT, gc + (size_t)k * SLOT };
-            }
-            stage2_kernel<<<dim3(nc * 64), 256, 0, stream>>>(sa);
+            for (int i = i_lo; i <= i_hi; ++i)
+                ma.cellorder[idx++] = i * 9 + (d - i);
         }
-    } else {
-        float* ws = (float*)d_ws;
-        for (int d = 0; d <= 16; ++d) {
-            const int i_lo = d > 8 ? d - 8 : 0;
-            const int i_hi = d < 8 ? d : 8;
-            const int nc = i_hi - i_lo + 1;
-            SegArgs base{}, inc{};
-            CellBatchArgs ca{};
-            int nb = 0, ni = 0;
-            for (int s = 0; s < nc; ++s) {
-                const int i = i_lo + s, j = d - i;
-                const int k = i * 9 + j;
-                float* oh = ws + (size_t)(2 * s) * SLOT;
-                float* oc = oh + SLOT;
-                const float* Wh = W_hp + (size_t)k * HID * W3;
-                const float* Wc = W_cp + (size_t)k * HID * W3;
-                base.d[nb++] = { grid_h + (size_t)k * SLOT, Wh, b_hp + (size_t)k * HID, oh, 512 };
-                base.d[nb++] = { grid_c + (size_t)k * SLOT, Wc, b_cp + (size_t)k * HID, oc, 512 };
-                if (i == 0 && j == 0) {
-                    inc.d[ni++] = { h_ext, Wh, nullptr, oh, 0 };
-                    inc.d[ni++] = { c_ext, Wc, nullptr, oc, 0 };
-                } else if (j > 0) {
-                    inc.d[ni++] = { gh + (size_t)(k - 1) * SLOT, Wh, nullptr, oh, 0 };
-                    inc.d[ni++] = { gc + (size_t)(k - 1) * SLOT, Wc, nullptr, oc, 0 };
-                }
-                if (i > 0) {
-                    inc.d[ni++] = { gh + (size_t)(k - 9) * SLOT, Wh, nullptr, oh, 256 };
-                    inc.d[ni++] = { gc + (size_t)(k - 9) * SLOT, Wc, nullptr, oc, 256 };
-                }
-                ca.d[s] = { oh, oc,
-                            W_hh + (size_t)k * 4 * HID * HID,
-                            W_ih + (size_t)k * 4 * HID,
-                            b_ih + (size_t)k * 4 * HID,
-                            b_hh + (size_t)k * 4 * HID,
-                            x + i * 9 + j,
-                            gh + (size_t)k * SLOT,
-                            gc + (size_t)k * SLOT };
-            }
-            projseg_kernel<<<dim3(8, 2, nb), 256, 0, stream>>>(base);
-            projseg_kernel<<<dim3(8, 2, ni), 256, 0, stream>>>(inc);
-            cell_kernel<<<dim3(8, 8, nc), 256, 0, stream>>>(ca);
-        }
-    }
+    }
+    mega_kernel<<<dim3(NBLK), 256, 0, stream>>>(ma);
+
     final_kernel<<<dim3(64), 256, 0, stream>>>(
         gh + (size_t)80 * SLOT, gc + (size_t)80 * SLOT,
         W_out, b_out, out, fh, fc);
```
